# Kernel optimization log

Measured on AMD Instinct MI355X. Metric: run time of the kernel, lower is better.

Reference implementation:

```python
import jax, jax.numpy as jnp
import numpy as np

N = 50000   # nodes (cells)
E = 800000  # directed edges
D = 512     # input/output feature dim (genes)
H = D // 64 # bottleneck dim = 8
LN_EPS = 1e-5


def setup_inputs() -> dict:
    key = jax.random.key(0)
    ks = jax.random.split(key, 6)
    x = jax.random.normal(ks[0], (N, D), dtype=jnp.float32)
    edge_index = jax.random.randint(ks[1], (2, E), 0, N, dtype=jnp.int64)
    size_factors = jax.random.uniform(ks[2], (N, 1), dtype=jnp.float32) + 0.5
    s1 = float(1.0 / np.sqrt(D))
    W1 = jax.random.uniform(ks[3], (D, H), jnp.float32, -s1, s1)
    b1 = jnp.zeros((H,), jnp.float32)
    gamma = jnp.ones((H,), jnp.float32)
    beta = jnp.zeros((H,), jnp.float32)
    s2 = float(1.0 / np.sqrt(H))
    W2 = jax.random.uniform(ks[4], (H, D), jnp.float32, -s2, s2)
    b2 = jnp.zeros((D,), jnp.float32)
    return {"x": x, "size_factors": size_factors, "W1": W1, "b1": b1,
            "gamma": gamma, "beta": beta, "W2": W2, "b2": b2,
            "edge_index": edge_index}


def _gcn_conv(x, W, b, src, dst, norm):
    # PyG GCNConv: linear transform, then sym-normalized scatter-add aggregation.
    h = x @ W                                   # [N, out]
    msg = h[src] * norm[:, None]                # [E+N, out] gather + scale
    out = jax.ops.segment_sum(msg, dst, num_segments=N)  # scatter-add
    return out + b


def reference(x, size_factors, W1, b1, gamma, beta, W2, b2, edge_index):
    loops = jnp.arange(N, dtype=edge_index.dtype)
    src = jnp.concatenate([edge_index[0], loops])  # add self-loops
    dst = jnp.concatenate([edge_index[1], loops])
    deg = jax.ops.segment_sum(jnp.ones_like(src, dtype=x.dtype), dst,
                              num_segments=N)       # deg >= 1 via self-loops
    dinv = jax.lax.rsqrt(deg)
    norm = dinv[src] * dinv[dst]                    # [E+N]

    h = _gcn_conv(x, W1, b1, src, dst, norm)        # [N, H]
    mu = jnp.mean(h, axis=-1, keepdims=True)
    var = jnp.var(h, axis=-1, keepdims=True)
    h = (h - mu) * jax.lax.rsqrt(var + LN_EPS) * gamma + beta
    h = jax.nn.relu(h)
    # dropout p=0.0 -> identity
    out = jax.nn.relu(_gcn_conv(h, W2, b2, src, dst, norm))  # [N, D]
    return out * size_factors
```

## Files before the change

kernel.cpp:

```cpp
#include <hip/hip_runtime.h>

#define NN 50000
#define EE 800000
#define DD 512
#define HH 8
#define BA 160
#define CHUNK 5000
#define NBIN 196
#define BCAP 4608
#define GBLK 782
#define NTILE 3125
#define AGBLK 1563

typedef short bf16x8 __attribute__((ext_vector_type(8)));
typedef float f32x4 __attribute__((ext_vector_type(4)));

union U16 { uint4 u; bf16x8 v; unsigned short h[8]; };

__device__ __forceinline__ unsigned short f2bf(float f) {
    union { float f; unsigned int i; } c; c.f = f;
    unsigned int i = c.i;
    i += 0x7fffu + ((i >> 16) & 1u);
    return (unsigned short)(i >> 16);
}

__global__ __launch_bounds__(256) void k_hist(const int* __restrict__ dst,
                                              int* __restrict__ blockhist) {
    __shared__ int h[256];
    int t = threadIdx.x, blk = blockIdx.x;
    h[t] = 0; __syncthreads();
    int base = blk * CHUNK;
#pragma unroll
    for (int it = 0; it < 20; ++it) {
        int i = it * 256 + t;
        if (i < CHUNK) atomicAdd(&h[dst[base + i] >> 8], 1);
    }
    __syncthreads();
    blockhist[blk * 256 + t] = h[t];
}

__global__ __launch_bounds__(256) void k_scan(int* __restrict__ blockhist,
                                              int* __restrict__ binBase,
                                              int* __restrict__ row) {
    __shared__ int s[256];
    int t = threadIdx.x;
    int sum = 0;
    for (int b = 0; b < BA; ++b) sum += blockhist[b * 256 + t];
    s[t] = sum; __syncthreads();
    for (int off = 1; off < 256; off <<= 1) {
        int x = (t >= off) ? s[t - off] : 0;
        __syncthreads();
        if (t >= off) s[t] += x;
        __syncthreads();
    }
    int excl = s[t] - sum;
    binBase[t] = excl;
    if (t == 255) { binBase[256] = s[255]; row[NN] = s[255]; }
    int run = excl;
    for (int b = 0; b < BA; ++b) {
        int v = blockhist[b * 256 + t];
        blockhist[b * 256 + t] = run;
        run += v;
    }
}

__global__ __launch_bounds__(256) void k_scatter(const int* __restrict__ eidx,
                                                 const int* __restrict__ blockhist,
                                                 int2* __restrict__ bucket) {
    __shared__ int cur[256];
    int t = threadIdx.x, blk = blockIdx.x;
    cur[t] = blockhist[blk * 256 + t]; __syncthreads();
    int base = blk * CHUNK;
#pragma unroll
    for (int it = 0; it < 20; ++it) {
        int i = it * 256 + t;
        if (i < CHUNK) {
            int s = eidx[base + i], d = eidx[EE + base + i];
            int pos = atomicAdd(&cur[d >> 8], 1);
            bucket[pos] = make_int2(s, d);
        }
    }
}

__global__ __launch_bounds__(256) void k_build_gemm1(const int2* __restrict__ bucket,
                                                     const int* __restrict__ binBase,
                                                     const float4* __restrict__ x4,
                                                     const float* __restrict__ W1,
                                                     int* __restrict__ row,
                                                     int* __restrict__ adj,
                                                     float* __restrict__ dinvA,
                                                     float* __restrict__ t1) {
    __shared__ int smem[11264];
    int t = threadIdx.x;
    if (blockIdx.x >= NBIN) {
        unsigned short* sbf = (unsigned short*)smem;
        for (int i = t; i < 16 * 64 * 8; i += 256) {
            int lane = (i >> 3) & 63, j = i & 7;
            int n = lane & 15;
            int k = (i >> 9) * 32 + ((lane >> 4) * 8) + j;
            sbf[i] = (n < HH) ? f2bf(W1[k * HH + n]) : (unsigned short)0;
        }
        __syncthreads();
        int wave = t >> 6, lane = t & 63;
        int tile = (blockIdx.x - NBIN) * 4 + wave;
        if (tile >= NTILE) return;
        int node0 = tile * 16;
        int m = lane & 15, q = lane >> 4;
        const float4* xrow = x4 + (size_t)(node0 + m) * (DD / 4) + q * 2;
        const uint4* bfrag = (const uint4*)sbf;
        f32x4 acc = {0.f, 0.f, 0.f, 0.f};
#pragma unroll
        for (int step = 0; step < 16; ++step) {
            float4 u0 = xrow[step * 8];
            float4 u1 = xrow[step * 8 + 1];
            U16 a, b;
            a.h[0] = f2bf(u0.x); a.h[1] = f2bf(u0.y); a.h[2] = f2bf(u0.z); a.h[3] = f2bf(u0.w);
            a.h[4] = f2bf(u1.x); a.h[5] = f2bf(u1.y); a.h[6] = f2bf(u1.z); a.h[7] = f2bf(u1.w);
            b.u = bfrag[step * 64 + lane];
            acc = __builtin_amdgcn_mfma_f32_16x16x32_bf16(a.v, b.v, acc, 0, 0, 0);
        }
        if (m < HH) {
            int base = (node0 + q * 4) * HH + m;
            t1[base]          = acc[0];
            t1[base + HH]     = acc[1];
            t1[base + 2 * HH] = acc[2];
            t1[base + 3 * HH] = acc[3];
        }
        return;
    }
    int bin = blockIdx.x;
    int n0 = bin << 8;
    int segStart = binBase[bin];
    int count = binBase[bin + 1] - segStart;
    if (count > BCAP) count = BCAP;
    int* lds_s   = smem;
    int* lds_out = smem + BCAP;
    int* cnt     = smem + 2 * BCAP;
    int* off     = smem + 2 * BCAP + 256;
    int* cur2    = smem + 2 * BCAP + 512;
    unsigned char* lds_d = (unsigned char*)(smem + 2 * BCAP + 768);
    cnt[t] = 0; __syncthreads();
    for (int i = t; i < count; i += 256) {
        int2 p = bucket[segStart + i];
        lds_s[i] = p.x;
        int dl = p.y - n0;
        lds_d[i] = (unsigned char)dl;
        atomicAdd(&cnt[dl], 1);
    }
    __syncthreads();
    off[t] = cnt[t]; __syncthreads();
    for (int o = 1; o < 256; o <<= 1) {
        int x = (t >= o) ? off[t - o] : 0;
        __syncthreads();
        if (t >= o) off[t] += x;
        __syncthreads();
    }
    int excl = off[t] - cnt[t];
    cur2[t] = excl;
    int n = n0 + t;
    if (n < NN) {
        row[n] = segStart + excl;
        dinvA[n] = rsqrtf((float)cnt[t] + 1.0f);
    }
    __syncthreads();
    for (int i = t; i < count; i += 256) {
        int pos = atomicAdd(&cur2[lds_d[i]], 1);
        lds_out[pos] = lds_s[i];
    }
    __syncthreads();
    for (int i = t; i < count; i += 256)
        adj[segStart + i] = lds_out[i];
}

__global__ __launch_bounds__(256) void k_agg1(const float* __restrict__ t1,
                                              const int* __restrict__ row,
                                              const int* __restrict__ adj,
                                              const float* __restrict__ dinvA,
                                              const float* __restrict__ b1,
                                              const float* __restrict__ gma,
                                              const float* __restrict__ bta,
                                              float* __restrict__ h2) {
    int gid = blockIdx.x * 256 + threadIdx.x;
    int n = gid >> 3, f = gid & 7;
    if (n >= NN) return;
    int beg = row[n], end = row[n + 1];
    float dv = dinvA[n];
    float acc = t1[(size_t)n * HH + f] * dv;
    int i = beg;
    for (; i + 2 <= end; i += 2) {
        int s0 = adj[i], s1 = adj[i + 1];
        float w0 = dinvA[s0], w1 = dinvA[s1];
        acc += t1[(size_t)s0 * HH + f] * w0;
        acc += t1[(size_t)s1 * HH + f] * w1;
    }
    if (i < end) {
        int s0 = adj[i];
        acc += t1[(size_t)s0 * HH + f] * dinvA[s0];
    }
    acc = acc * dv + b1[f];
    float s = acc;
    s += __shfl_xor(s, 1); s += __shfl_xor(s, 2); s += __shfl_xor(s, 4);
    float mu = s * 0.125f;
    float dx = acc - mu;
    float sq = dx * dx;
    sq += __shfl_xor(sq, 1); sq += __shfl_xor(sq, 2); sq += __shfl_xor(sq, 4);
    float rs = rsqrtf(sq * 0.125f + 1e-5f);
    h2[(size_t)n * HH + f] = fmaxf(dx * rs * gma[f] + bta[f], 0.f);
}

__global__ __launch_bounds__(256) void k_agg2_gemm2(const float* __restrict__ h2,
                                                    const int* __restrict__ row,
                                                    const int* __restrict__ adj,
                                                    const float* __restrict__ dinvA,
                                                    const float* __restrict__ W2,
                                                    const float* __restrict__ b2,
                                                    const float* __restrict__ sf,
                                                    float* __restrict__ out) {
    __shared__ float sA[32 * 8];
    int tid = threadIdx.x;
    int c = tid & 63, g = tid >> 6, d0 = c * 8;
    float w[8][8];
#pragma unroll
    for (int k = 0; k < 8; ++k) {
        float4 u0 = *(const float4*)(W2 + k * DD + d0);
        float4 u1 = *(const float4*)(W2 + k * DD + d0 + 4);
        w[k][0] = u0.x; w[k][1] = u0.y; w[k][2] = u0.z; w[k][3] = u0.w;
        w[k][4] = u1.x; w[k][5] = u1.y; w[k][6] = u1.z; w[k][7] = u1.w;
    }
    float bb[8];
    {
        float4 u0 = *(const float4*)(b2 + d0);
        float4 u1 = *(const float4*)(b2 + d0 + 4);
        bb[0] = u0.x; bb[1] = u0.y; bb[2] = u0.z; bb[3] = u0.w;
        bb[4] = u1.x; bb[5] = u1.y; bb[6] = u1.z; bb[7] = u1.w;
    }
    int nl = tid >> 3, f = tid & 7;
    int n = blockIdx.x * 32 + nl;
    if (n < NN) {
        int beg = row[n], end = row[n + 1];
        float dv = dinvA[n];
        float acc = h2[(size_t)n * HH + f] * dv;
        int i = beg;
        for (; i + 2 <= end; i += 2) {
            int s0 = adj[i], s1 = adj[i + 1];
            float w0 = dinvA[s0], w1 = dinvA[s1];
            acc += h2[(size_t)s0 * HH + f] * w0;
            acc += h2[(size_t)s1 * HH + f] * w1;
        }
        if (i < end) {
            int s0 = adj[i];
            acc += h2[(size_t)s0 * HH + f] * dinvA[s0];
        }
        sA[nl * 8 + f] = acc * dv;
    }
    __syncthreads();
#pragma unroll
    for (int i = 0; i < 8; ++i) {
        int rrow = i * 4 + g;
        int n2 = blockIdx.x * 32 + rrow;
        if (n2 < NN) {
            float a[8];
#pragma unroll
            for (int j = 0; j < 8; ++j) a[j] = sA[rrow * 8 + j];
            float s = sf[n2];
            float acc[8];
#pragma unroll
            for (int j = 0; j < 8; ++j) acc[j] = bb[j];
#pragma unroll
            for (int k = 0; k < 8; ++k)
#pragma unroll
                for (int j = 0; j < 8; ++j) acc[j] += a[k] * w[k][j];
            float4 o0 = make_float4(fmaxf(acc[0], 0.f) * s, fmaxf(acc[1], 0.f) * s,
                                    fmaxf(acc[2], 0.f) * s, fmaxf(acc[3], 0.f) * s);
            float4 o1 = make_float4(fmaxf(acc[4], 0.f) * s, fmaxf(acc[5], 0.f) * s,
                                    fmaxf(acc[6], 0.f) * s, fmaxf(acc[7], 0.f) * s);
            float4* op = (float4*)(out + (size_t)n2 * DD + d0);
            op[0] = o0;
            op[1] = o1;
        }
    }
}

extern "C" void kernel_launch(void* const* d_in, const int* in_sizes, int n_in,
                              void* d_out, int out_size, void* d_ws, size_t ws_size,
                              hipStream_t stream) {
    (void)in_sizes; (void)n_in; (void)out_size; (void)ws_size;
    const float* x   = (const float*)d_in[0];
    const float* sf  = (const float*)d_in[1];
    const float* W1  = (const float*)d_in[2];
    const float* b1  = (const float*)d_in[3];
    const float* gma = (const float*)d_in[4];
    const float* bta = (const float*)d_in[5];
    const float* W2  = (const float*)d_in[6];
    const float* b2  = (const float*)d_in[7];
    const int* eidx  = (const int*)d_in[8];
    float* out = (float*)d_out;

    char* ws = (char*)d_ws;
    int*   blockhist = (int*)(ws + 0);
    int*   binBase   = (int*)(ws + 262144);
    int*   row       = (int*)(ws + (1 << 20));
    float* dinvA     = (float*)(ws + 2 * (1 << 20));
    float* t1        = (float*)(ws + 3 * (1 << 20));
    float* h2        = (float*)(ws + 5 * (1 << 20));
    int*   adj       = (int*)(ws + 7 * (1 << 20));
    int2*  bucket    = (int2*)(ws + 11 * (1 << 20));

    k_hist<<<BA, 256, 0, stream>>>(eidx + EE, blockhist);
    k_scan<<<1, 256, 0, stream>>>(blockhist, binBase, row);
    k_scatter<<<BA, 256, 0, stream>>>(eidx, blockhist, bucket);
    k_build_gemm1<<<NBIN + GBLK, 256, 0, stream>>>(bucket, binBase, (const float4*)x,
                                                   W1, row, adj, dinvA, t1);
    k_agg1<<<AGBLK, 256, 0, stream>>>(t1, row, adj, dinvA, b1, gma, bta, h2);
    k_agg2_gemm2<<<AGBLK, 256, 0, stream>>>(h2, row, adj, dinvA, W2, b2, sf, out);
}
```

Measured before the change: 285.2 us.

## Fuse GEMM1 with histogram, pack bucket entries, double-buffer x loads

Moves the x@W1 MFMA GEMM out of the build kernel and co-schedules it with the destination histogram in one launch. The build kernel becomes smaller and uses less LDS. Bucket entries are packed into one int, (src<<8)|local dst, which halves the scatter write and build read traffic. The GEMM loop now uses explicit two-buffer register prefetch of x rows to overlap loads with MFMA. Packing relies on src<<8 fitting in 32 bits, which holds for N=50000. The extra prefetch registers may reduce occupancy.

```diff
diff --git a/kernel.cpp b/kernel.cpp
--- a/kernel.cpp
+++ b/kernel.cpp
@@ -24,19 +24,80 @@
     return (unsigned short)(i >> 16);
 }
 
-__global__ __launch_bounds__(256) void k_hist(const int* __restrict__ dst,
-                                              int* __restrict__ blockhist) {
-    __shared__ int h[256];
-    int t = threadIdx.x, blk = blockIdx.x;
-    h[t] = 0; __syncthreads();
-    int base = blk * CHUNK;
-#pragma unroll
-    for (int it = 0; it < 20; ++it) {
-        int i = it * 256 + t;
-        if (i < CHUNK) atomicAdd(&h[dst[base + i] >> 8], 1);
-    }
-    __syncthreads();
-    blockhist[blk * 256 + t] = h[t];
+__global__ __launch_bounds__(256) void k_gemm1_hist(const float4* __restrict__ x4,
+                                                    const float* __restrict__ W1,
+                                                    const int* __restrict__ dst,
+                                                    float* __restrict__ t1,
+                                                    int* __restrict__ blockhist) {
+    __shared__ int smem[4096];
+    int t = threadIdx.x;
+    if (blockIdx.x >= GBLK) {
+        int blk = blockIdx.x - GBLK;
+        int* h = smem;
+        h[t] = 0; __syncthreads();
+        int base = blk * CHUNK;
+#pragma unroll
+        for (int it = 0; it < 20; ++it) {
+            int i = it * 256 + t;
+            if (i < CHUNK) atomicAdd(&h[dst[base + i] >> 8], 1);
+        }
+        __syncthreads();
+        blockhist[blk * 256 + t] = h[t];
+        return;
+    }
+    unsigned short* sbf = (unsigned short*)smem;
+    for (int i = t; i < 16 * 64 * 8; i += 256) {
+        int lane = (i >> 3) & 63, j = i & 7;
+        int n = lane & 15;
+        int k = (i >> 9) * 32 + ((lane >> 4) * 8) + j;
+        sbf[i] = (n < HH) ? f2bf(W1[k * HH + n]) : (unsigned short)0;
+    }
+    __syncthreads();
+    int wave = t >> 6, lane = t & 63;
+    int tile = blockIdx.x * 4 + wave;
+    if (tile >= NTILE) return;
+    int node0 = tile * 16;
+    int m = lane & 15, q = lane >> 4;
+    const float4* xrow = x4 + (size_t)(node0 + m) * (DD / 4) + q * 2;
+    const uint4* bfrag = (const uint4*)sbf;
+    f32x4 acc = {0.f, 0.f, 0.f, 0.f};
+
+    float4 bufA[8], bufB[8];
+#define LOADG(buf, g)                                                      \
+    _Pragma("unroll")                                                      \
+    for (int s = 0; s < 4; ++s) {                                          \
+        buf[2 * s]     = xrow[((g) * 4 + s) * 8];                          \
+        buf[2 * s + 1] = xrow[((g) * 4 + s) * 8 + 1];                      \
+    }
+#define MFMAG(buf, g)                                                      \
+    _Pragma("unroll")                                                      \
+    for (int s = 0; s < 4; ++s) {                                          \
+        U16 a, b;                                                          \
+        float4 u0 = buf[2 * s], u1 = buf[2 * s + 1];                       \
+        a.h[0] = f2bf(u0.x); a.h[1] = f2bf(u0.y);                          \
+        a.h[2] = f2bf(u0.z); a.h[3] = f2bf(u0.w);                          \
+        a.h[4] = f2bf(u1.x); a.h[5] = f2bf(u1.y);                          \
+        a.h[6] = f2bf(u1.z); a.h[7] = f2bf(u1.w);                          \
+        b.u = bfrag[((g) * 4 + s) * 64 + lane];                            \
+        acc = __builtin_amdgcn_mfma_f32_16x16x32_bf16(a.v, b.v, acc, 0, 0, 0); \
+    }
+    LOADG(bufA, 0)
+    LOADG(bufB, 1)
+    MFMAG(bufA, 0)
+    LOADG(bufA, 2)
+    MFMAG(bufB, 1)
+    LOADG(bufB, 3)
+    MFMAG(bufA, 2)
+    MFMAG(bufB, 3)
+#undef LOADG
+#undef MFMAG
+    if (m < HH) {
+        int base = (node0 + q * 4) * HH + m;
+        t1[base]          = acc[0];
+        t1[base + HH]     = acc[1];
+        t1[base + 2 * HH] = acc[2];
+        t1[base + 3 * HH] = acc[3];
+    }
 }
 
 __global__ __launch_bounds__(256) void k_scan(int* __restrict__ blockhist,
@@ -66,7 +127,7 @@
 
 __global__ __launch_bounds__(256) void k_scatter(const int* __restrict__ eidx,
                                                  const int* __restrict__ blockhist,
-                                                 int2* __restrict__ bucket) {
+                                                 int* __restrict__ bucket) {
     __shared__ int cur[256];
     int t = threadIdx.x, blk = blockIdx.x;
     cur[t] = blockhist[blk * 256 + t]; __syncthreads();
@@ -77,75 +138,33 @@
         if (i < CHUNK) {
             int s = eidx[base + i], d = eidx[EE + base + i];
             int pos = atomicAdd(&cur[d >> 8], 1);
-            bucket[pos] = make_int2(s, d);
-        }
-    }
-}
-
-__global__ __launch_bounds__(256) void k_build_gemm1(const int2* __restrict__ bucket,
-                                                     const int* __restrict__ binBase,
-                                                     const float4* __restrict__ x4,
-                                                     const float* __restrict__ W1,
-                                                     int* __restrict__ row,
-                                                     int* __restrict__ adj,
-                                                     float* __restrict__ dinvA,
-                                                     float* __restrict__ t1) {
-    __shared__ int smem[11264];
+            bucket[pos] = (s << 8) | (d & 255);
+        }
+    }
+}
+
+__global__ __launch_bounds__(256) void k_build(const int* __restrict__ bucket,
+                                               const int* __restrict__ binBase,
+                                               int* __restrict__ row,
+                                               int* __restrict__ adj,
+                                               float* __restrict__ dinvA) {
+    __shared__ int smem[2 * BCAP + 768];
     int t = threadIdx.x;
-    if (blockIdx.x >= NBIN) {
-        unsigned short* sbf = (unsigned short*)smem;
-        for (int i = t; i < 16 * 64 * 8; i += 256) {
-            int lane = (i >> 3) & 63, j = i & 7;
-            int n = lane & 15;
-            int k = (i >> 9) * 32 + ((lane >> 4) * 8) + j;
-            sbf[i] = (n < HH) ? f2bf(W1[k * HH + n]) : (unsigned short)0;
-        }
-        __syncthreads();
-        int wave = t >> 6, lane = t & 63;
-        int tile = (blockIdx.x - NBIN) * 4 + wave;
-        if (tile >= NTILE) return;
-        int node0 = tile * 16;
-        int m = lane & 15, q = lane >> 4;
-        const float4* xrow = x4 + (size_t)(node0 + m) * (DD / 4) + q * 2;
-        const uint4* bfrag = (const uint4*)sbf;
-        f32x4 acc = {0.f, 0.f, 0.f, 0.f};
-#pragma unroll
-        for (int step = 0; step < 16; ++step) {
-            float4 u0 = xrow[step * 8];
-            float4 u1 = xrow[step * 8 + 1];
-            U16 a, b;
-            a.h[0] = f2bf(u0.x); a.h[1] = f2bf(u0.y); a.h[2] = f2bf(u0.z); a.h[3] = f2bf(u0.w);
-            a.h[4] = f2bf(u1.x); a.h[5] = f2bf(u1.y); a.h[6] = f2bf(u1.z); a.h[7] = f2bf(u1.w);
-            b.u = bfrag[step * 64 + lane];
-            acc = __builtin_amdgcn_mfma_f32_16x16x32_bf16(a.v, b.v, acc, 0, 0, 0);
-        }
-        if (m < HH) {
-            int base = (node0 + q * 4) * HH + m;
-            t1[base]          = acc[0];
-            t1[base + HH]     = acc[1];
-            t1[base + 2 * HH] = acc[2];
-            t1[base + 3 * HH] = acc[3];
-        }
-        return;
-    }
     int bin = blockIdx.x;
     int n0 = bin << 8;
     int segStart = binBase[bin];
     int count = binBase[bin + 1] - segStart;
     if (count > BCAP) count = BCAP;
-    int* lds_s   = smem;
+    int* lds_in  = smem;
     int* lds_out = smem + BCAP;
     int* cnt     = smem + 2 * BCAP;
     int* off     = smem + 2 * BCAP + 256;
     int* cur2    = smem + 2 * BCAP + 512;
-    unsigned char* lds_d = (unsigned char*)(smem + 2 * BCAP + 768);
     cnt[t] = 0; __syncthreads();
     for (int i = t; i < count; i += 256) {
-        int2 p = bucket[segStart + i];
-        lds_s[i] = p.x;
-        int dl = p.y - n0;
-        lds_d[i] = (unsigned char)dl;
-        atomicAdd(&cnt[dl], 1);
+        int p = bucket[segStart + i];
+        lds_in[i] = p;
+        atomicAdd(&cnt[p & 255], 1);
     }
     __syncthreads();
     off[t] = cnt[t]; __syncthreads();
@@ -164,8 +183,9 @@
     }
     __syncthreads();
     for (int i = t; i < count; i += 256) {
-        int pos = atomicAdd(&cur2[lds_d[i]], 1);
-        lds_out[pos] = lds_s[i];
+        int p = lds_in[i];
+        int pos = atomicAdd(&cur2[p & 255], 1);
+        lds_out[pos] = p >> 8;
     }
     __syncthreads();
     for (int i = t; i < count; i += 256)
@@ -304,13 +324,13 @@
     float* t1        = (float*)(ws + 3 * (1 << 20));
     float* h2        = (float*)(ws + 5 * (1 << 20));
     int*   adj       = (int*)(ws + 7 * (1 << 20));
-    int2*  bucket    = (int2*)(ws + 11 * (1 << 20));
-
-    k_hist<<<BA, 256, 0, stream>>>(eidx + EE, blockhist);
+    int*   bucket    = (int*)(ws + 11 * (1 << 20));
+
+    k_gemm1_hist<<<GBLK + BA, 256, 0, stream>>>((const float4*)x, W1, eidx + EE,
+                                                t1, blockhist);
     k_scan<<<1, 256, 0, stream>>>(blockhist, binBase, row);
     k_scatter<<<BA, 256, 0, stream>>>(eidx, blockhist, bucket);
-    k_build_gemm1<<<NBIN + GBLK, 256, 0, stream>>>(bucket, binBase, (const float4*)x,
-                                                   W1, row, adj, dinvA, t1);
+    k_build<<<NBIN, 256, 0, stream>>>(bucket, binBase, row, adj, dinvA);
     k_agg1<<<AGBLK, 256, 0, stream>>>(t1, row, adj, dinvA, b1, gma, bta, h2);
     k_agg2_gemm2<<<AGBLK, 256, 0, stream>>>(h2, row, adj, dinvA, W2, b2, sf, out);
 }
```

New measurement: 282.5 us. Within noise of the previous version (-0.9%).
